# Performance work log

Hardware: AMD Instinct MI355X
Metric: run time of the kernel (lower is better)

Reference implementation:

```python
import jax, jax.numpy as jnp
import numpy as np

NUM_GROUPS = 8
EPS = 1e-5


def group_norm(x, scale, bias):
    # x: [b, c, h, w]; 8 groups, affine, eps=1e-5 (torch GroupNorm defaults)
    b, c, h, w = x.shape
    xg = x.reshape(b, NUM_GROUPS, c // NUM_GROUPS * h * w)
    mean = jnp.mean(xg, axis=-1, keepdims=True)
    var = jnp.var(xg, axis=-1, keepdims=True)
    xg = (xg - mean) * jax.lax.rsqrt(var + EPS)
    x = xg.reshape(b, c, h, w)
    return x * scale[None, :, None, None] + bias[None, :, None, None]


def conv1x1(x, w, bias):
    # 1x1 conv == per-pixel linear: x [b,c,h,w], w [c_out,c_in], bias [c_out]
    return jnp.einsum('oc,bchw->bohw', w, x) + bias[None, :, None, None]


def setup_inputs() -> dict:
    key = jax.random.key(0)
    ks = jax.random.split(key, 11)
    b, c, h, w = 8, 512, 32, 32
    init = 1.0 / np.sqrt(c)
    d = {
        'x': jax.random.normal(ks[0], (b, c, h, w), dtype=jnp.float32),
        'gn_scale': jnp.ones((c,), jnp.float32),
        'gn_bias': jnp.zeros((c,), jnp.float32),
        'wq': jax.random.uniform(ks[1], (c, c), jnp.float32, -init, init),
        'bq': jax.random.uniform(ks[2], (c,), jnp.float32, -init, init),
        'wk': jax.random.uniform(ks[3], (c, c), jnp.float32, -init, init),
        'bk': jax.random.uniform(ks[4], (c,), jnp.float32, -init, init),
        'wv': jax.random.uniform(ks[5], (c, c), jnp.float32, -init, init),
        'bv': jax.random.uniform(ks[6], (c,), jnp.float32, -init, init),
        'wproj': jax.random.uniform(ks[7], (c, c), jnp.float32, -init, init),
        'bproj': jax.random.uniform(ks[8], (c,), jnp.float32, -init, init),
    }
    return d


def reference(x, gn_scale, gn_bias, wq, bq, wk, bk, wv, bv, wproj, bproj):
    b, c, h, w = x.shape
    h_ = group_norm(x, gn_scale, gn_bias)
    q = conv1x1(h_, wq, bq).reshape(b, c, h * w)  # [b,c,hw]
    k = conv1x1(h_, wk, bk).reshape(b, c, h * w)
    v = conv1x1(h_, wv, bv).reshape(b, c, h * w)
    scale = 1.0 / np.sqrt(c).astype(np.float32)
    # scores[b,i,j] = sum_c q[b,c,i]*k[b,c,j]
    scores = jnp.einsum('bci,bcj->bij', q, k) * scale
    attn = jax.nn.softmax(scores, axis=2)  # softmax over j (keys)
    # h_[b,c,i] = sum_j v[b,c,j] * attn[b,i,j]
    out = jnp.einsum('bcj,bij->bci', v, attn).reshape(b, c, h, w)
    out = conv1x1(out, wproj, bproj)
    return x + out
```

## Files before the change

kernel.cpp:

```cpp
#include <hip/hip_runtime.h>
#include <hip/hip_bf16.h>

#define DI __device__ __forceinline__

typedef __bf16 bf16x8 __attribute__((ext_vector_type(8)));
typedef float f32x4 __attribute__((ext_vector_type(4)));

typedef const void __attribute__((address_space(1))) gas_t;
typedef void __attribute__((address_space(3))) las_t;

DI unsigned short f2bf(float f) {
    unsigned u = __builtin_bit_cast(unsigned, f);
    u += 0x7fffu + ((u >> 16) & 1u);
    return (unsigned short)(u >> 16);
}

template <int ROWS>
DI void stage_tile(const unsigned short* __restrict__ g, int ldK,
                   unsigned short* lds, int t) {
    int row_in = t >> 3;
    int kg = (t & 7) ^ (row_in & 7);
    const unsigned short* src = g + (size_t)row_in * ldK + kg * 8;
    unsigned short* dst = lds + ((t >> 6) << 9);
#pragma unroll
    for (int c = 0; c < ROWS / 32; ++c) {
        __builtin_amdgcn_global_load_lds(
            (gas_t*)(unsigned long long)(src + (size_t)c * 32 * ldK),
            (las_t*)(unsigned)(unsigned long long)(dst + c * 2048),
            16, 0, 0);
    }
}

DI bf16x8 frag(const unsigned short* lds, int r, int kg) {
    return *(const bf16x8*)((const char*)lds + r * 128 + ((kg ^ (r & 7)) << 4));
}

template <int MR>
DI void compute_step(const unsigned short* As_, const unsigned short* Bs_,
                     f32x4 (&acc)[MR][4], int wm, int wn, int l15, int lks) {
#pragma unroll
    for (int kk = 0; kk < 2; ++kk) {
        bf16x8 a_[MR], b_[4];
#pragma unroll
        for (int m = 0; m < MR; ++m) a_[m] = frag(As_, wm + m * 16 + l15, kk * 4 + lks);
#pragma unroll
        for (int n = 0; n < 4; ++n) b_[n] = frag(Bs_, wn + n * 16 + l15, kk * 4 + lks);
#pragma unroll
        for (int m = 0; m < MR; ++m)
#pragma unroll
            for (int n = 0; n < 4; ++n)
                acc[m][n] = __builtin_amdgcn_mfma_f32_16x16x32_bf16(a_[m], b_[n], acc[m][n], 0, 0, 0);
    }
}

template <int TM, int MODE, int PIPE>
DI void gemm_phase(unsigned short* AsB, unsigned short* BsB,
                   const unsigned short* __restrict__ A, const unsigned short* __restrict__ B,
                   const float* __restrict__ b0, const float* __restrict__ b1,
                   const float* __restrict__ b2,
                   void* __restrict__ C0, void* __restrict__ C1, void* __restrict__ C2,
                   const float* __restrict__ resid, float* __restrict__ spart,
                   int M, int N, int K, float scale, size_t sA, size_t sB, size_t sC,
                   int bx, int t) {
    constexpr int MR = TM / 32;
    constexpr int ABUF = TM * 64;
    constexpr int BBUF = 128 * 64;
    int b = bx & 7;
    int tile = bx >> 3;
    int nTx = N >> 7;
    int tx = tile % nTx, ty = tile / nTx;
    int m0 = ty * TM, n0 = tx << 7;
    const unsigned short* Ag = A + sA * b + (size_t)m0 * K;
    const unsigned short* Bg = B + sB * b + (size_t)n0 * K;
    int lane = t & 63, wid = t >> 6;
    int wm = (wid >> 1) * (TM / 2), wn = (wid & 1) * 64;
    const int l15 = lane & 15, lks = lane >> 4;
    const int rbase = lks * 4;

    f32x4 acc[MR][4];
#pragma unroll
    for (int i = 0; i < MR; ++i)
#pragma unroll
        for (int j = 0; j < 4; ++j) acc[i][j] = (f32x4){0.f, 0.f, 0.f, 0.f};

    float inv[4];
    if constexpr (MODE == 2) {
#pragma unroll
        for (int n = 0; n < 4; ++n) {
            int ng = n0 + wn + n * 16 + l15;
            float ssum = 0.f;
#pragma unroll
            for (int k = 0; k < 16; ++k) ssum += spart[(size_t)(b * 16 + k) * 1024 + ng];
            inv[n] = 1.f / ssum;
        }
    }
    float bn4[4];
    if constexpr (MODE == 3) {
#pragma unroll
        for (int n = 0; n < 4; ++n) bn4[n] = b0[n0 + wn + n * 16 + l15];
    }

    if constexpr (PIPE == 0) {
        for (int k0 = 0; k0 < K; k0 += 64) {
            stage_tile<TM>(Ag + k0, K, AsB, t);
            stage_tile<128>(Bg + k0, K, BsB, t);
            asm volatile("s_waitcnt vmcnt(0)" ::: "memory");
            __syncthreads();
            compute_step<MR>(AsB, BsB, acc, wm, wn, l15, lks);
            __syncthreads();
        }
    } else {
        stage_tile<TM>(Ag, K, AsB, t);
        stage_tile<128>(Bg, K, BsB, t);
        asm volatile("s_waitcnt vmcnt(0)" ::: "memory");
        __syncthreads();
        int cur = 0;
        for (int k0 = 0; k0 < K; k0 += 64) {
            if (k0 + 64 < K) {
                stage_tile<TM>(Ag + k0 + 64, K, AsB + (cur ^ 1) * ABUF, t);
                stage_tile<128>(Bg + k0 + 64, K, BsB + (cur ^ 1) * BBUF, t);
            }
            compute_step<MR>(AsB + cur * ABUF, BsB + cur * BBUF, acc, wm, wn, l15, lks);
            if (k0 + 64 < K) {
                asm volatile("s_waitcnt vmcnt(0)" ::: "memory");
                __syncthreads();
            }
            cur ^= 1;
        }
    }

    const size_t cb = sC * b;
    if constexpr (MODE == 0) {
#pragma unroll
        for (int m = 0; m < MR; ++m) {
            int mgg = m0 + wm + m * 16 + rbase;
            int region = mgg >> 9;
            int local = mgg & 511;
            const float* bias = (region == 0) ? b0 : (region == 1) ? b1 : b2;
            float bv4[4];
#pragma unroll
            for (int j = 0; j < 4; ++j) bv4[j] = bias[local + j];
            if (region < 2) {
                unsigned short* Ct = (unsigned short*)(region == 0 ? C0 : C1) + cb;
#pragma unroll
                for (int n = 0; n < 4; ++n) {
                    int ng = n0 + wn + n * 16 + l15;
                    f32x4 v = acc[m][n];
                    ushort4 o;
                    o.x = f2bf(v[0] + bv4[0]); o.y = f2bf(v[1] + bv4[1]);
                    o.z = f2bf(v[2] + bv4[2]); o.w = f2bf(v[3] + bv4[3]);
                    *(ushort4*)&Ct[(size_t)ng * 512 + local] = o;
                }
            } else {
                unsigned short* Vb = (unsigned short*)C2 + cb;
#pragma unroll
                for (int n = 0; n < 4; ++n) {
                    int ng = n0 + wn + n * 16 + l15;
                    f32x4 v = acc[m][n];
#pragma unroll
                    for (int j = 0; j < 4; ++j)
                        Vb[(size_t)(local + j) * 1024 + ng] = f2bf(v[j] + bv4[j]);
                }
            }
        }
    } else if constexpr (MODE == 1) {
        unsigned short* Eb = (unsigned short*)C0 + cb;
        int part = tx * 2 + (wid & 1);
#pragma unroll
        for (int m = 0; m < MR; ++m) {
            float ps[4] = {0.f, 0.f, 0.f, 0.f};
#pragma unroll
            for (int n = 0; n < 4; ++n) {
                int jg = n0 + wn + n * 16 + l15;
                f32x4 v = acc[m][n];
#pragma unroll
                for (int jr = 0; jr < 4; ++jr) {
                    float e = __expf(v[jr] * scale);
                    ps[jr] += e;
                    int row = m0 + wm + m * 16 + rbase + jr;
                    Eb[(size_t)row * N + jg] = f2bf(e);
                }
            }
#pragma unroll
            for (int jr = 0; jr < 4; ++jr) {
                float p = ps[jr];
                p += __shfl_xor(p, 1); p += __shfl_xor(p, 2);
                p += __shfl_xor(p, 4); p += __shfl_xor(p, 8);
                if (l15 == 0) {
                    int row = m0 + wm + m * 16 + rbase + jr;
                    spart[(size_t)(b * 16 + part) * 1024 + row] = p;
                }
            }
        }
    } else if constexpr (MODE == 2) {
        unsigned short* Ct = (unsigned short*)C0 + cb;
#pragma unroll
        for (int m = 0; m < MR; ++m) {
            int mg = m0 + wm + m * 16 + rbase;
#pragma unroll
            for (int n = 0; n < 4; ++n) {
                int ng = n0 + wn + n * 16 + l15;
                f32x4 v = acc[m][n];
                ushort4 o;
                o.x = f2bf(v[0] * inv[n]); o.y = f2bf(v[1] * inv[n]);
                o.z = f2bf(v[2] * inv[n]); o.w = f2bf(v[3] * inv[n]);
                *(ushort4*)&Ct[(size_t)ng * M + mg] = o;
            }
        }
    } else {
        float* Cf = (float*)C0 + cb;
#pragma unroll
        for (int m = 0; m < MR; ++m) {
            int mg = m0 + wm + m * 16 + rbase;
#pragma unroll
            for (int n = 0; n < 4; ++n) {
                int ng = n0 + wn + n * 16 + l15;
                f32x4 v = acc[m][n];
                const float* rp = resid + cb + (size_t)ng * M + mg;
                float4 o;
                o.x = v[0] + bn4[n] + rp[0]; o.y = v[1] + bn4[n] + rp[1];
                o.z = v[2] + bn4[n] + rp[2]; o.w = v[3] + bn4[n] + rp[3];
                *(float4*)&Cf[(size_t)ng * M + mg] = o;
            }
        }
    }
}

DI void stats_body(const float* __restrict__ x, float2* __restrict__ part,
                   float* red, int bx, int t) {
    int b = bx & 7, g = (bx >> 3) & 7, ch = bx >> 6;
    size_t base = ((size_t)b * 512 + g * 64 + ch * 8) * 1024;
    const float4* xp = (const float4*)(x + base);
    float s = 0.f, q = 0.f;
#pragma unroll
    for (int it = 0; it < 8; ++it) {
        float4 v = xp[it * 256 + t];
        s += (v.x + v.y) + (v.z + v.w);
        q += (v.x * v.x + v.y * v.y) + (v.z * v.z + v.w * v.w);
    }
#pragma unroll
    for (int o = 32; o; o >>= 1) { s += __shfl_xor(s, o); q += __shfl_xor(q, o); }
    int lane = t & 63, wid = t >> 6;
    if (!lane) { red[wid] = s; red[4 + wid] = q; }
    __syncthreads();
    if (t == 0)
        part[((b * 8 + g) * 8) + ch] =
            make_float2(red[0] + red[1] + red[2] + red[3],
                        red[4] + red[5] + red[6] + red[7]);
}

__global__ __launch_bounds__(256) void prep_kernel(const float* __restrict__ x,
                                                   float2* __restrict__ part,
                                                   const float* __restrict__ w0,
                                                   const float* __restrict__ w1,
                                                   const float* __restrict__ w2,
                                                   const float* __restrict__ w3,
                                                   unsigned short* __restrict__ wb) {
    __shared__ float red[8];
    int bx = blockIdx.x, t = threadIdx.x;
    if (bx < 512) {
        stats_body(x, part, red, bx, t);
    } else {
        int chunk = bx - 512;
        int w = chunk >> 8;
        const float* sp = (w == 0) ? w0 : (w == 1) ? w1 : (w == 2) ? w2 : w3;
        unsigned short* o = wb + (size_t)w * 262144;
        int idx = (chunk & 255) * 256 + t;
        float4 v = ((const float4*)sp)[idx];
        ushort4 r;
        r.x = f2bf(v.x); r.y = f2bf(v.y); r.z = f2bf(v.z); r.w = f2bf(v.w);
        ((ushort4*)o)[idx] = r;
    }
}

__global__ __launch_bounds__(256) void gn_applyT(const float* __restrict__ x,
                                                 const float2* __restrict__ part,
                                                 const float* __restrict__ gs,
                                                 const float* __restrict__ gb,
                                                 unsigned short* __restrict__ hT) {
    __shared__ unsigned short tile[128 * 66];
    int bx = blockIdx.x, t = threadIdx.x;
    int b = bx & 7, g = (bx >> 3) & 7, ic = bx >> 6;
    int bg = b * 8 + g;
    float s = 0.f, q = 0.f;
#pragma unroll
    for (int k = 0; k < 8; ++k) { float2 p = part[bg * 8 + k]; s += p.x; q += p.y; }
    float mean = s * (1.f / 65536.f);
    float var = q * (1.f / 65536.f) - mean * mean;
    float rstd = rsqrtf(var + 1e-5f);

    int i4 = t & 31, cq = t >> 5;
    size_t xbase = ((size_t)b * 512 + g * 64) * 1024 + ic * 128;
#pragma unroll
    for (int pass = 0; pass < 8; ++pass) {
        int c = pass * 8 + cq;
        float4 v = *(const float4*)&x[xbase + (size_t)c * 1024 + i4 * 4];
        int gc = g * 64 + c;
        float sc = gs[gc] * rstd, bi = gb[gc] - mean * sc;
        unsigned short* tp = &tile[(i4 * 4) * 66 + c];
        tp[0]   = f2bf(v.x * sc + bi);
        tp[66]  = f2bf(v.y * sc + bi);
        tp[132] = f2bf(v.z * sc + bi);
        tp[198] = f2bf(v.w * sc + bi);
    }
    __syncthreads();
    int i = t >> 1, h = t & 1;
    const unsigned short* tp2 = &tile[i * 66 + h * 32];
    unsigned short* op = &hT[(size_t)b * (1024 * 512) + (size_t)(ic * 128 + i) * 512 + g * 64 + h * 32];
#pragma unroll
    for (int cc = 0; cc < 4; ++cc) {
        unsigned short tmp[8];
#pragma unroll
        for (int j = 0; j < 8; ++j) tmp[j] = tp2[cc * 8 + j];
        *(uint4*)&op[cc * 8] = *(const uint4*)tmp;
    }
}

template <int TM, int MODE, int MINW, int PIPE>
__global__ __launch_bounds__(256, MINW) void gemm_bt(
        const unsigned short* __restrict__ A, const unsigned short* __restrict__ B,
        const float* __restrict__ b0, const float* __restrict__ b1,
        const float* __restrict__ b2,
        void* __restrict__ C0, void* __restrict__ C1, void* __restrict__ C2,
        const float* __restrict__ resid, float* __restrict__ spart,
        int M, int N, int K, float scale, size_t sA, size_t sB, size_t sC) {
    constexpr int NBUF = PIPE ? 2 : 1;
    __shared__ __align__(16) unsigned short As[NBUF * TM * 64];
    __shared__ __align__(16) unsigned short Bs[NBUF * 128 * 64];
    gemm_phase<TM, MODE, PIPE>(As, Bs, A, B, b0, b1, b2, C0, C1, C2, resid, spart,
                               M, N, K, scale, sA, sB, sC, blockIdx.x, threadIdx.x);
}

extern "C" void kernel_launch(void* const* d_in, const int* in_sizes, int n_in,
                              void* d_out, int out_size, void* d_ws, size_t ws_size,
                              hipStream_t stream) {
    const float* x  = (const float*)d_in[0];
    const float* gs = (const float*)d_in[1];
    const float* gb = (const float*)d_in[2];
    const float* wq = (const float*)d_in[3];
    const float* bq = (const float*)d_in[4];
    const float* wk = (const float*)d_in[5];
    const float* bk = (const float*)d_in[6];
    const float* wv = (const float*)d_in[7];
    const float* bv = (const float*)d_in[8];
    const float* wp = (const float*)d_in[9];
    const float* bp = (const float*)d_in[10];
    float* out = (float*)d_out;

    char* ws = (char*)d_ws;
    const size_t MB = 1u << 20;
    unsigned short* hT = (unsigned short*)(ws + 0);
    unsigned short* wb = (unsigned short*)(ws + 8 * MB);
    unsigned short* qT = (unsigned short*)(ws + 10 * MB);
    unsigned short* kT = (unsigned short*)(ws + 18 * MB);
    unsigned short* vN = (unsigned short*)(ws + 26 * MB);
    unsigned short* E  = (unsigned short*)(ws + 34 * MB);
    unsigned short* OT = (unsigned short*)(ws + 50 * MB);
    float2* gnpart     = (float2*)(ws + 58 * MB);
    float*  spart      = (float*)(ws + 58 * MB + 65536);

    const unsigned short* wpb = wb + 3 * 262144;
    const size_t sH = 1024 * 512;
    const size_t sS = 1024 * 1024;

    prep_kernel<<<1536, 256, 0, stream>>>(x, gnpart, wq, wk, wv, wp, wb);
    gn_applyT<<<512, 256, 0, stream>>>(x, gnpart, gs, gb, hT);

    gemm_bt<128, 0, 3, 0><<<768, 256, 0, stream>>>(
        wb, hT, bq, bk, bv, qT, kT, vN, nullptr, nullptr,
        1536, 1024, 512, 1.f, 0, sH, sH);
    gemm_bt<128, 1, 2, 1><<<512, 256, 0, stream>>>(
        qT, kT, nullptr, nullptr, nullptr, E, nullptr, nullptr, nullptr, spart,
        1024, 1024, 512, 0.044194173824159216f, sH, sH, sS);
    gemm_bt<64, 2, 2, 1><<<512, 256, 0, stream>>>(
        vN, E, nullptr, nullptr, nullptr, OT, nullptr, nullptr, nullptr, spart,
        512, 1024, 1024, 1.f, sH, sS, sH);
    gemm_bt<64, 3, 2, 1><<<512, 256, 0, stream>>>(
        OT, wpb, bp, nullptr, nullptr, out, nullptr, nullptr, x, nullptr,
        1024, 512, 512, 1.f, sH, 0, sH);
}
```

Baseline: 76.85 us.

## Fuse QK^T, softmax and PV into a single flash-style attention kernel

Replaces the separate scores/exp GEMM and the PV GEMM with one kernel that computes exp scores per 64-key tile in LDS and accumulates P·V directly, normalizing by row sums at the end. This removes the large bf16 exp matrix and partial-sum buffers written to and read from global memory, plus one launch. In exchange each block processes 32 queries with one block per CU, no load/compute overlap, and repeatedly restages K and V, so occupancy and latency hiding are low.

```diff
diff --git a/kernel.cpp b/kernel.cpp
--- a/kernel.cpp
+++ b/kernel.cpp
@@ -31,8 +31,26 @@
     }
 }
 
+DI void stage_v32(const unsigned short* __restrict__ g, unsigned short* lds, int t) {
+    int row = t >> 2;
+    int s = t & 3;
+    int kg = s ^ (row & 3);
+    const unsigned short* src = g + (size_t)row * 1024 + kg * 8;
+    unsigned short* dst = lds + ((t >> 6) << 9);
+#pragma unroll
+    for (int c = 0; c < 8; ++c) {
+        __builtin_amdgcn_global_load_lds(
+            (gas_t*)(unsigned long long)(src + (size_t)c * 64 * 1024),
+            (las_t*)(unsigned)(unsigned long long)(dst + c * 2048),
+            16, 0, 0);
+    }
+}
+
 DI bf16x8 frag(const unsigned short* lds, int r, int kg) {
     return *(const bf16x8*)((const char*)lds + r * 128 + ((kg ^ (r & 7)) << 4));
+}
+DI bf16x8 fragV(const unsigned short* lds, int c, int j8) {
+    return *(const bf16x8*)((const char*)lds + c * 64 + ((j8 ^ (c & 3)) << 4));
 }
 
 template <int MR>
@@ -51,6 +69,129 @@
             for (int n = 0; n < 4; ++n)
                 acc[m][n] = __builtin_amdgcn_mfma_f32_16x16x32_bf16(a_[m], b_[n], acc[m][n], 0, 0, 0);
     }
+}
+
+__global__ __launch_bounds__(256, 1) void attn_fused(
+        const unsigned short* __restrict__ qT, const unsigned short* __restrict__ kT,
+        const unsigned short* __restrict__ vN, unsigned short* __restrict__ OT) {
+    __shared__ __align__(16) unsigned short Qs[32 * 512];
+    __shared__ __align__(16) unsigned short Ks[64 * 512];
+    __shared__ __align__(16) unsigned short Vs[512 * 32];
+    __shared__ __align__(16) unsigned short Ps[32 * 64];
+    __shared__ float red[4 * 32];
+    int bx = blockIdx.x, t = threadIdx.x;
+    int b = bx & 7;
+    int i0 = (bx >> 3) << 5;
+    int lane = t & 63, w = t >> 6;
+    const int l15 = lane & 15, lks = lane >> 4;
+    const int rbase = lks * 4;
+    const size_t sH = 1024 * 512;
+    const unsigned short* Qg = qT + sH * b + (size_t)i0 * 512;
+    const unsigned short* Kg = kT + sH * b;
+    const unsigned short* Vg = vN + sH * b;
+    const float scale = 0.044194173824159216f;
+
+#pragma unroll
+    for (int kc = 0; kc < 8; ++kc)
+        stage_tile<32>(Qg + kc * 64, 512, Qs + kc * 2048, t);
+
+    f32x4 oacc[2][8];
+#pragma unroll
+    for (int m = 0; m < 2; ++m)
+#pragma unroll
+        for (int n = 0; n < 8; ++n) oacc[m][n] = (f32x4){0.f, 0.f, 0.f, 0.f};
+    float rs[2][4] = {{0.f, 0.f, 0.f, 0.f}, {0.f, 0.f, 0.f, 0.f}};
+
+    for (int j0 = 0; j0 < 1024; j0 += 64) {
+#pragma unroll
+        for (int kc = 0; kc < 8; ++kc)
+            stage_tile<64>(Kg + (size_t)j0 * 512 + kc * 64, 512, Ks + kc * 4096, t);
+        stage_v32(Vg + j0, Vs, t);
+        asm volatile("s_waitcnt vmcnt(0)" ::: "memory");
+        __syncthreads();
+
+        f32x4 eacc[2];
+        eacc[0] = (f32x4){0.f, 0.f, 0.f, 0.f};
+        eacc[1] = (f32x4){0.f, 0.f, 0.f, 0.f};
+#pragma unroll
+        for (int kc = 0; kc < 8; ++kc) {
+#pragma unroll
+            for (int sub = 0; sub < 2; ++sub) {
+                int slot = sub * 4 + lks;
+                bf16x8 bk = frag(Ks + kc * 4096, w * 16 + l15, slot);
+                eacc[0] = __builtin_amdgcn_mfma_f32_16x16x32_bf16(
+                    frag(Qs + kc * 2048, l15, slot), bk, eacc[0], 0, 0, 0);
+                eacc[1] = __builtin_amdgcn_mfma_f32_16x16x32_bf16(
+                    frag(Qs + kc * 2048, 16 + l15, slot), bk, eacc[1], 0, 0, 0);
+            }
+        }
+#pragma unroll
+        for (int m = 0; m < 2; ++m) {
+#pragma unroll
+            for (int jr = 0; jr < 4; ++jr) {
+                int i = m * 16 + rbase + jr;
+                int j = w * 16 + l15;
+                float e = __expf(eacc[m][jr] * scale);
+                Ps[i * 64 + (((j >> 3) ^ (i & 7)) << 3) + (j & 7)] = f2bf(e);
+                float p = e;
+                p += __shfl_xor(p, 1); p += __shfl_xor(p, 2);
+                p += __shfl_xor(p, 4); p += __shfl_xor(p, 8);
+                rs[m][jr] += p;
+            }
+        }
+        __syncthreads();
+
+#pragma unroll
+        for (int n = 0; n < 8; ++n) {
+            bf16x8 bv = fragV(Vs, w * 128 + n * 16 + l15, lks);
+            oacc[0][n] = __builtin_amdgcn_mfma_f32_16x16x32_bf16(
+                frag(Ps, l15, lks), bv, oacc[0][n], 0, 0, 0);
+            oacc[1][n] = __builtin_amdgcn_mfma_f32_16x16x32_bf16(
+                frag(Ps, 16 + l15, lks), bv, oacc[1][n], 0, 0, 0);
+        }
+        __syncthreads();
+        stage_v32(Vg + j0 + 32, Vs, t);
+        asm volatile("s_waitcnt vmcnt(0)" ::: "memory");
+        __syncthreads();
+#pragma unroll
+        for (int n = 0; n < 8; ++n) {
+            bf16x8 bv = fragV(Vs, w * 128 + n * 16 + l15, lks);
+            oacc[0][n] = __builtin_amdgcn_mfma_f32_16x16x32_bf16(
+                frag(Ps, l15, 4 + lks), bv, oacc[0][n], 0, 0, 0);
+            oacc[1][n] = __builtin_amdgcn_mfma_f32_16x16x32_bf16(
+                frag(Ps, 16 + l15, 4 + lks), bv, oacc[1][n], 0, 0, 0);
+        }
+        __syncthreads();
+    }
+
+    if (l15 == 0) {
+#pragma unroll
+        for (int m = 0; m < 2; ++m)
+#pragma unroll
+            for (int jr = 0; jr < 4; ++jr)
+                red[w * 32 + m * 16 + rbase + jr] = rs[m][jr];
+    }
+    __syncthreads();
+    float inv[2][4];
+#pragma unroll
+    for (int m = 0; m < 2; ++m)
+#pragma unroll
+        for (int jr = 0; jr < 4; ++jr) {
+            int i = m * 16 + rbase + jr;
+            inv[m][jr] = 1.f / (red[i] + red[32 + i] + red[64 + i] + red[96 + i]);
+        }
+    unsigned short* Ob = OT + sH * b;
+#pragma unroll
+    for (int m = 0; m < 2; ++m)
+#pragma unroll
+        for (int n = 0; n < 8; ++n) {
+            int c = w * 128 + n * 16 + l15;
+#pragma unroll
+            for (int jr = 0; jr < 4; ++jr) {
+                int i = i0 + m * 16 + rbase + jr;
+                Ob[(size_t)i * 512 + c] = f2bf(oacc[m][n][jr] * inv[m][jr]);
+            }
+        }
 }
 
 template <int TM, int MODE, int PIPE>
@@ -59,8 +200,8 @@
                    const float* __restrict__ b0, const float* __restrict__ b1,
                    const float* __restrict__ b2,
                    void* __restrict__ C0, void* __restrict__ C1, void* __restrict__ C2,
-                   const float* __restrict__ resid, float* __restrict__ spart,
-                   int M, int N, int K, float scale, size_t sA, size_t sB, size_t sC,
+                   const float* __restrict__ resid,
+                   int M, int N, int K, size_t sA, size_t sB, size_t sC,
                    int bx, int t) {
     constexpr int MR = TM / 32;
     constexpr int ABUF = TM * 64;
@@ -83,17 +224,6 @@
 #pragma unroll
         for (int j = 0; j < 4; ++j) acc[i][j] = (f32x4){0.f, 0.f, 0.f, 0.f};
 
-    float inv[4];
-    if constexpr (MODE == 2) {
-#pragma unroll
-        for (int n = 0; n < 4; ++n) {
-            int ng = n0 + wn + n * 16 + l15;
-            float ssum = 0.f;
-#pragma unroll
-            for (int k = 0; k < 16; ++k) ssum += spart[(size_t)(b * 16 + k) * 1024 + ng];
-            inv[n] = 1.f / ssum;
-        }
-    }
     float bn4[4];
     if constexpr (MODE == 3) {
 #pragma unroll
@@ -161,50 +291,6 @@
                     for (int j = 0; j < 4; ++j)
                         Vb[(size_t)(local + j) * 1024 + ng] = f2bf(v[j] + bv4[j]);
                 }
-            }
-        }
-    } else if constexpr (MODE == 1) {
-        unsigned short* Eb = (unsigned short*)C0 + cb;
-        int part = tx * 2 + (wid & 1);
-#pragma unroll
-        for (int m = 0; m < MR; ++m) {
-            float ps[4] = {0.f, 0.f, 0.f, 0.f};
-#pragma unroll
-            for (int n = 0; n < 4; ++n) {
-                int jg = n0 + wn + n * 16 + l15;
-                f32x4 v = acc[m][n];
-#pragma unroll
-                for (int jr = 0; jr < 4; ++jr) {
-                    float e = __expf(v[jr] * scale);
-                    ps[jr] += e;
-                    int row = m0 + wm + m * 16 + rbase + jr;
-                    Eb[(size_t)row * N + jg] = f2bf(e);
-                }
-            }
-#pragma unroll
-            for (int jr = 0; jr < 4; ++jr) {
-                float p = ps[jr];
-                p += __shfl_xor(p, 1); p += __shfl_xor(p, 2);
-                p += __shfl_xor(p, 4); p += __shfl_xor(p, 8);
-                if (l15 == 0) {
-                    int row = m0 + wm + m * 16 + rbase + jr;
-                    spart[(size_t)(b * 16 + part) * 1024 + row] = p;
-                }
-            }
-        }
-    } else if constexpr (MODE == 2) {
-        unsigned short* Ct = (unsigned short*)C0 + cb;
-#pragma unroll
-        for (int m = 0; m < MR; ++m) {
-            int mg = m0 + wm + m * 16 + rbase;
-#pragma unroll
-            for (int n = 0; n < 4; ++n) {
-                int ng = n0 + wn + n * 16 + l15;
-                f32x4 v = acc[m][n];
-                ushort4 o;
-                o.x = f2bf(v[0] * inv[n]); o.y = f2bf(v[1] * inv[n]);
-                o.z = f2bf(v[2] * inv[n]); o.w = f2bf(v[3] * inv[n]);
-                *(ushort4*)&Ct[(size_t)ng * M + mg] = o;
             }
         }
     } else {
@@ -322,13 +408,13 @@
         const float* __restrict__ b0, const float* __restrict__ b1,
         const float* __restrict__ b2,
         void* __restrict__ C0, void* __restrict__ C1, void* __restrict__ C2,
-        const float* __restrict__ resid, float* __restrict__ spart,
-        int M, int N, int K, float scale, size_t sA, size_t sB, size_t sC) {
+        const float* __restrict__ resid,
+        int M, int N, int K, size_t sA, size_t sB, size_t sC) {
     constexpr int NBUF = PIPE ? 2 : 1;
     __shared__ __align__(16) unsigned short As[NBUF * TM * 64];
     __shared__ __align__(16) unsigned short Bs[NBUF * 128 * 64];
-    gemm_phase<TM, MODE, PIPE>(As, Bs, A, B, b0, b1, b2, C0, C1, C2, resid, spart,
-                               M, N, K, scale, sA, sB, sC, blockIdx.x, threadIdx.x);
+    gemm_phase<TM, MODE, PIPE>(As, Bs, A, B, b0, b1, b2, C0, C1, C2, resid,
+                               M, N, K, sA, sB, sC, blockIdx.x, threadIdx.x);
 }
 
 extern "C" void kernel_launch(void* const* d_in, const int* in_sizes, int n_in,
@@ -354,28 +440,20 @@
     unsigned short* qT = (unsigned short*)(ws + 10 * MB);
     unsigned short* kT = (unsigned short*)(ws + 18 * MB);
     unsigned short* vN = (unsigned short*)(ws + 26 * MB);
-    unsigned short* E  = (unsigned short*)(ws + 34 * MB);
-    unsigned short* OT = (unsigned short*)(ws + 50 * MB);
-    float2* gnpart     = (float2*)(ws + 58 * MB);
-    float*  spart      = (float*)(ws + 58 * MB + 65536);
+    unsigned short* OT = (unsigned short*)(ws + 34 * MB);
+    float2* gnpart     = (float2*)(ws + 42 * MB);
 
     const unsigned short* wpb = wb + 3 * 262144;
     const size_t sH = 1024 * 512;
-    const size_t sS = 1024 * 1024;
 
     prep_kernel<<<1536, 256, 0, stream>>>(x, gnpart, wq, wk, wv, wp, wb);
     gn_applyT<<<512, 256, 0, stream>>>(x, gnpart, gs, gb, hT);
 
     gemm_bt<128, 0, 3, 0><<<768, 256, 0, stream>>>(
-        wb, hT, bq, bk, bv, qT, kT, vN, nullptr, nullptr,
-        1536, 1024, 512, 1.f, 0, sH, sH);
-    gemm_bt<128, 1, 2, 1><<<512, 256, 0, stream>>>(
-        qT, kT, nullptr, nullptr, nullptr, E, nullptr, nullptr, nullptr, spart,
-        1024, 1024, 512, 0.044194173824159216f, sH, sH, sS);
-    gemm_bt<64, 2, 2, 1><<<512, 256, 0, stream>>>(
-        vN, E, nullptr, nullptr, nullptr, OT, nullptr, nullptr, nullptr, spart,
-        512, 1024, 1024, 1.f, sH, sS, sH);
+        wb, hT, bq, bk, bv, qT, kT, vN, nullptr,
+        1536, 1024, 512, 0, sH, sH);
+    attn_fused<<<256, 256, 0, stream>>>(qT, kT, vN, OT);
     gemm_bt<64, 3, 2, 1><<<512, 256, 0, stream>>>(
-        OT, wpb, bp, nullptr, nullptr, out, nullptr, nullptr, x, nullptr,
-        1024, 512, 512, 1.f, sH, 0, sH);
-}
+        OT, wpb, bp, nullptr, nullptr, out, nullptr, nullptr, x,
+        1024, 512, 512, sH, 0, sH);
+}
```

New measurement: 105.7 us. +37.5%, slower.
